# Kernel tuning notes

Hardware: AMD Instinct MI355X
Metric: run time of the kernel (lower is better)

Reference implementation:

```python
import jax, jax.numpy as jnp
import numpy as np

L, H, D, HD, DFF, V, S, B = 12, 12, 768, 64, 3072, 50257, 512, 4
NEG = -1e10  # mask value used by the torch module (applied incl. diagonal, pre-scale)


def layer_norm(x, g, b, eps=1e-5):
    u = jnp.mean(x, axis=-1, keepdims=True)
    v = jnp.mean((x - u) ** 2, axis=-1, keepdims=True)  # biased variance
    return g * (x - u) / jnp.sqrt(v + eps) + b


def setup_inputs() -> dict:
    key = jax.random.key(0)
    ks = jax.random.split(key, 10)
    f = lambda k, s: 0.02 * jax.random.normal(k, s, dtype=jnp.float32)
    return {
        "tokens": jax.random.randint(ks[0], (B, S), 0, V),
        "E": f(ks[1], (V, D)),
        "P": f(ks[2], (S, D)),
        "Wq": f(ks[3], (L, H, HD, D)),
        "Wk": f(ks[4], (L, H, HD, D)),
        "Wv": f(ks[5], (L, H, HD, D)),
        "Wo": f(ks[6], (L, D, D)),
        "bo": jnp.zeros((L, D), jnp.float32),
        "g1": jnp.ones((L, D), jnp.float32),
        "b1": jnp.zeros((L, D), jnp.float32),
        "g2": jnp.ones((L, D), jnp.float32),
        "b2": jnp.zeros((L, D), jnp.float32),
        "W1": f(ks[7], (L, DFF, D)),
        "bff1": jnp.zeros((L, DFF), jnp.float32),
        "W2": f(ks[8], (L, D, DFF)),
        "bff2": jnp.zeros((L, D), jnp.float32),
        "gf": jnp.ones((D,), jnp.float32),
        "bf": jnp.zeros((D,), jnp.float32),
    }


def reference(tokens, E, P, Wq, Wk, Wv, Wo, bo, g1, b1, g2, b2, W1, bff1, W2, bff2, gf, bf):
    x = E[tokens] + P[None, :, :]  # [B,S,D]; embed_dropout is identity at eval
    # Faithful mask: triu with diagonal=0 (masks the diagonal too), added BEFORE 1/sqrt(dk)
    mask = jnp.triu(jnp.ones((S, S), jnp.float32), k=0) * NEG
    scale = 1.0 / jnp.sqrt(jnp.float32(HD))
    for l in range(L):
        h = layer_norm(x, g1[l], b1[l])
        Q = jnp.einsum('bsd,hkd->bhsk', h, Wq[l])
        K = jnp.einsum('bsd,hkd->bhsk', h, Wk[l])
        Vh = jnp.einsum('bsd,hkd->bhsk', h, Wv[l])
        sc = (jnp.einsum('bhqk,bhmk->bhqm', Q, K) + mask) * scale  # [B,H,S,S]
        A = jax.nn.softmax(sc, axis=-1)
        o = jnp.einsum('bhqm,bhmk->bhqk', A, Vh)  # [B,H,S,HD]
        o = o.transpose(0, 2, 1, 3).reshape(B, S, D)  # concat heads
        x = x + jnp.einsum('bsd,ed->bse', o, Wo[l]) + bo[l]
        h2 = layer_norm(x, g2[l], b2[l])
        ff = jax.nn.gelu(jnp.einsum('bsd,fd->bsf', h2, W1[l]) + bff1[l], approximate=False)
        x = x + jnp.einsum('bsf,df->bsd', ff, W2[l]) + bff2[l]
    x = layer_norm(x, gf, bf)
    return jnp.einsum('bsd,vd->bsv', x, E)  # weight-tied LM head
```

## Files before the change

kernel.cpp:

```cpp
#include <hip/hip_runtime.h>
#include <hip/hip_bf16.h>
#include <math.h>
#include <stdint.h>

#define L      12
#define H      12
#define DMODEL 768
#define HDIM   64
#define DFF    3072
#define VOCAB  50257
#define VPAD2  50432
#define SEQ    512
#define BATCH  4
#define MTOK   2048
#define BKK    64

typedef __hip_bfloat16 bf16;
typedef __bf16 bf16x8 __attribute__((ext_vector_type(8)));
typedef float  f32x4  __attribute__((ext_vector_type(4)));

__device__ inline unsigned int f2bf_bits(float f) {
    __hip_bfloat16 h = __float2bfloat16(f);
    return (unsigned int)__builtin_bit_cast(unsigned short, h);
}

typedef __attribute__((address_space(1))) unsigned int as1_uint;
typedef __attribute__((address_space(3))) unsigned int as3_uint;

__device__ inline void load_lds_16B(const void* g, void* l) {
    __builtin_amdgcn_global_load_lds((as1_uint*)(uintptr_t)g,
                                     (as3_uint*)(uintptr_t)l, 16, 0, 0);
}

__device__ inline int xcd_swz(int raw, int nwg) {
    return (raw & 7) * (nwg >> 3) + (raw >> 3);
}

struct CvtP {
    const float* src[7];
    bf16* dst[7];
    long ns[7];
    long nt[7];
};

__global__ void cvt_all_kernel(CvtP c) {
    long gid0 = ((long)blockIdx.x * blockDim.x + threadIdx.x) * 8;
    long gstr = (long)gridDim.x * blockDim.x * 8;
    for (int s = 0; s < 7; s++) {
        const float* src = c.src[s];
        bf16* dst = c.dst[s];
        long ns = c.ns[s], ntt = c.nt[s];
        for (long i8 = gid0; i8 < ntt; i8 += gstr) {
            uint4 out;
            if (i8 < ns) {
                float4 a = *reinterpret_cast<const float4*>(src + i8);
                float4 b = *reinterpret_cast<const float4*>(src + i8 + 4);
                out.x = f2bf_bits(a.x) | (f2bf_bits(a.y) << 16);
                out.y = f2bf_bits(a.z) | (f2bf_bits(a.w) << 16);
                out.z = f2bf_bits(b.x) | (f2bf_bits(b.y) << 16);
                out.w = f2bf_bits(b.z) | (f2bf_bits(b.w) << 16);
            } else {
                out = (uint4){0u, 0u, 0u, 0u};
            }
            *reinterpret_cast<uint4*>(dst + i8) = out;
        }
    }
}

__global__ __launch_bounds__(256) void embed_ln_kernel(
        float* __restrict__ x, bf16* __restrict__ hout,
        const int* __restrict__ tok, const float* __restrict__ E,
        const float* __restrict__ Pp, const float* __restrict__ g,
        const float* __restrict__ b) {
    int wave = threadIdx.x >> 6, lane = threadIdx.x & 63;
    int row = blockIdx.x * 4 + wave;
    int s = row & (SEQ - 1);
    long ebase = (long)tok[row] * 192;
    const float4* E4 = (const float4*)E;
    const float4* P4 = (const float4*)Pp;
    float4 v[3];
    float s1 = 0.f, s2 = 0.f;
    #pragma unroll
    for (int e = 0; e < 3; e++) {
        int c4 = e * 64 + lane;
        float4 a = E4[ebase + c4];
        float4 p = P4[s * 192 + c4];
        a.x += p.x; a.y += p.y; a.z += p.z; a.w += p.w;
        v[e] = a;
        ((float4*)x)[(size_t)row * 192 + c4] = a;
        s1 += a.x + a.y + a.z + a.w;
        s2 += a.x * a.x + a.y * a.y + a.z * a.z + a.w * a.w;
    }
    #pragma unroll
    for (int o = 32; o > 0; o >>= 1) {
        s1 += __shfl_xor(s1, o);
        s2 += __shfl_xor(s2, o);
    }
    float u    = s1 * (1.f / DMODEL);
    float var  = s2 * (1.f / DMODEL) - u * u;
    float rstd = rsqrtf(var + 1e-5f);
    #pragma unroll
    for (int e = 0; e < 3; e++) {
        int c4 = e * 64 + lane;
        float4 gg = ((const float4*)g)[c4];
        float4 bb = ((const float4*)b)[c4];
        float y0 = gg.x * (v[e].x - u) * rstd + bb.x;
        float y1 = gg.y * (v[e].y - u) * rstd + bb.y;
        float y2 = gg.z * (v[e].z - u) * rstd + bb.z;
        float y3 = gg.w * (v[e].w - u) * rstd + bb.w;
        uint2 o2;
        o2.x = f2bf_bits(y0) | (f2bf_bits(y1) << 16);
        o2.y = f2bf_bits(y2) | (f2bf_bits(y3) << 16);
        ((uint2*)hout)[(size_t)row * 192 + c4] = o2;
    }
}

__global__ __launch_bounds__(256) void ln_kernel(
        const float* __restrict__ x, const float* __restrict__ g,
        const float* __restrict__ b, bf16* __restrict__ hout) {
    int wave = threadIdx.x >> 6, lane = threadIdx.x & 63;
    int row = blockIdx.x * 4 + wave;
    float4 v[3];
    float s1 = 0.f, s2 = 0.f;
    #pragma unroll
    for (int e = 0; e < 3; e++) {
        int c4 = e * 64 + lane;
        float4 a = ((const float4*)x)[(size_t)row * 192 + c4];
        v[e] = a;
        s1 += a.x + a.y + a.z + a.w;
        s2 += a.x * a.x + a.y * a.y + a.z * a.z + a.w * a.w;
    }
    #pragma unroll
    for (int o = 32; o > 0; o >>= 1) {
        s1 += __shfl_xor(s1, o);
        s2 += __shfl_xor(s2, o);
    }
    float u    = s1 * (1.f / DMODEL);
    float var  = s2 * (1.f / DMODEL) - u * u;
    float rstd = rsqrtf(var + 1e-5f);
    #pragma unroll
    for (int e = 0; e < 3; e++) {
        int c4 = e * 64 + lane;
        float4 gg = ((const float4*)g)[c4];
        float4 bb = ((const float4*)b)[c4];
        float y0 = gg.x * (v[e].x - u) * rstd + bb.x;
        float y1 = gg.y * (v[e].y - u) * rstd + bb.y;
        float y2 = gg.z * (v[e].z - u) * rstd + bb.z;
        float y3 = gg.w * (v[e].w - u) * rstd + bb.w;
        uint2 o2;
        o2.x = f2bf_bits(y0) | (f2bf_bits(y1) << 16);
        o2.y = f2bf_bits(y2) | (f2bf_bits(y3) << 16);
        ((uint2*)hout)[(size_t)row * 192 + c4] = o2;
    }
}

#define BM 128

template<int BN_, int EPI>
__global__ __launch_bounds__(256) void gemm_bt(
    const bf16* __restrict__ A, const bf16* __restrict__ Bmat, long strideBz,
    void* __restrict__ Cout, long strideCz,
    const float* __restrict__ bias,
    int Mm, int Nn, int Kk, int Nstore)
{
    constexpr int NF = BN_ / 32;
    __shared__ __align__(16) bf16 As[2][BM * BKK];
    __shared__ __align__(16) bf16 Bs[2][BN_ * BKK];
    int tid = threadIdx.x;
    int lane = tid & 63, wave = tid >> 6;

    int Mtiles = Mm / BM;
    int id = xcd_swz(blockIdx.x, gridDim.x);
    int bm = (id % Mtiles) * BM;
    int bn = (id / Mtiles) * BN_;
    int z = blockIdx.z;
    const bf16* Bz = Bmat + (size_t)z * strideBz;
    int wr = (wave >> 1) * 64, wc = (wave & 1) * (BN_ / 2);

    int nt = Kk / BKK;

    f32x4 acc[4][NF];
    #pragma unroll
    for (int i = 0; i < 4; i++)
        #pragma unroll
        for (int j = 0; j < NF; j++) acc[i][j] = (f32x4){0.f, 0.f, 0.f, 0.f};

    auto stage = [&](int slot, int kt) {
        #pragma unroll
        for (int i = 0; i < 4; i++) {
            int byte = i * 4096 + tid * 16;
            int r = byte >> 7;
            int scb = (byte & 127) ^ ((r & 7) << 4);
            load_lds_16B(A + (size_t)(bm + r) * Kk + kt + (scb >> 1),
                         (char*)As[slot] + byte);
        }
        #pragma unroll
        for (int i = 0; i < BN_ / 32; i++) {
            int byte = i * 4096 + tid * 16;
            int r = byte >> 7;
            int scb = (byte & 127) ^ ((r & 7) << 4);
            load_lds_16B(Bz + (size_t)(bn + r) * Kk + kt + (scb >> 1),
                         (char*)Bs[slot] + byte);
        }
    };

    const int swz_rd = (lane & 7) << 4;
    stage(0, 0);
    for (int t = 0; t < nt; ++t) {
        if (t + 1 < nt) {
            stage((t + 1) & 1, (t + 1) * BKK);
            if constexpr (BN_ == 128) {
                asm volatile("s_waitcnt vmcnt(8)" ::: "memory");
            } else {
                asm volatile("s_waitcnt vmcnt(6)" ::: "memory");
            }
        } else {
            asm volatile("s_waitcnt vmcnt(0)" ::: "memory");
        }
        __builtin_amdgcn_s_barrier();
        __builtin_amdgcn_sched_barrier(0);
        __builtin_amdgcn_s_setprio(1);
        int cur = t & 1;
        #pragma unroll
        for (int kk = 0; kk < 2; ++kk) {
            bf16x8 af[4], bfr[NF];
            int ro = lane & 15;
            int cob = kk * 64 + (lane >> 4) * 16;
            #pragma unroll
            for (int mi = 0; mi < 4; mi++) {
                int row = wr + mi * 16 + ro;
                af[mi] = *reinterpret_cast<const bf16x8*>(
                    (const char*)As[cur] + row * 128 + (cob ^ swz_rd));
            }
            #pragma unroll
            for (int ni = 0; ni < NF; ni++) {
                int row = wc + ni * 16 + ro;
                bfr[ni] = *reinterpret_cast<const bf16x8*>(
                    (const char*)Bs[cur] + row * 128 + (cob ^ swz_rd));
            }
            #pragma unroll
            for (int mi = 0; mi < 4; mi++)
                #pragma unroll
                for (int ni = 0; ni < NF; ni++)
                    acc[mi][ni] = __builtin_amdgcn_mfma_f32_16x16x32_bf16(
                        af[mi], bfr[ni], acc[mi][ni], 0, 0, 0);
        }
        __builtin_amdgcn_s_setprio(0);
        __builtin_amdgcn_s_barrier();
    }

    int rbase = bm + wr + ((lane >> 4) << 2);
    int cbase = bn + wc + (lane & 15);
    #pragma unroll
    for (int mi = 0; mi < 4; mi++) {
        #pragma unroll
        for (int ni = 0; ni < NF; ni++) {
            int col = cbase + ni * 16;
            #pragma unroll
            for (int r = 0; r < 4; r++) {
                int row = rbase + mi * 16 + r;
                float v = acc[mi][ni][r];
                if constexpr (EPI == 0) {
                    ((bf16*)Cout)[(size_t)z * strideCz + (size_t)row * Nn + col] =
                        __float2bfloat16(v);
                } else if constexpr (EPI == 1) {
                    size_t idx = (size_t)row * Nn + col;
                    float* resid = (float*)Cout;
                    resid[idx] = resid[idx] + v + bias[col];
                } else if constexpr (EPI == 2) {
                    float t2 = v + bias[col];
                    float gel = 0.5f * t2 * (1.f + erff(t2 * 0.70710678118654752f));
                    ((bf16*)Cout)[(size_t)row * Nn + col] = __float2bfloat16(gel);
                } else {
                    if (col < Nstore)
                        ((float*)Cout)[(size_t)row * Nstore + col] = v;
                }
            }
        }
    }
}

#define NEGMASK -1e10f
#define SM_SCALE 0.125f

__global__ __launch_bounds__(256) void attn_kernel(
    bf16* __restrict__ o, const bf16* __restrict__ qb,
    const bf16* __restrict__ kb, const bf16* __restrict__ vb)
{
    __shared__ __align__(16) bf16 K_lds[64 * 64];
    __shared__ __align__(16) bf16 VT_lds[64 * 64];
    __shared__ __align__(16) bf16 P_lds[4][16 * 64];

    int tid = threadIdx.x;
    int wave = tid >> 6, lane = tid & 63;
    int g = lane >> 4;
    int cq = lane & 15;
    int idx = xcd_swz(blockIdx.x, gridDim.x);
    int qt = idx & 7;
    int bh = idx >> 3;
    int h = bh % H, b = bh / H;
    int q0 = qt * 64;
    const size_t base = ((size_t)b * SEQ) * DMODEL + h * HDIM;

    bf16x8 qa[2];
    #pragma unroll
    for (int kk = 0; kk < 2; kk++)
        qa[kk] = *reinterpret_cast<const bf16x8*>(
            qb + base + (size_t)(q0 + wave * 16 + cq) * DMODEL + kk * 32 + g * 8);

    f32x4 acc_o[4];
    #pragma unroll
    for (int df = 0; df < 4; df++) acc_o[df] = (f32x4){0.f, 0.f, 0.f, 0.f};
    float m_run[4] = {-INFINITY, -INFINITY, -INFINITY, -INFINITY};
    float l_run[4] = {0.f, 0.f, 0.f, 0.f};

    int ntiles = (qt == 0) ? (SEQ / 64) : (qt + 1);
    for (int t = 0; t < ntiles; ++t) {
        int mt = t * 64;
        __syncthreads();
        #pragma unroll
        for (int i = 0; i < 2; i++) {
            int byte = i * 4096 + tid * 16;
            int r = byte >> 7;
            int scb = (byte & 127) ^ ((r & 7) << 4);
            load_lds_16B(kb + base + (size_t)(mt + r) * DMODEL + (scb >> 1),
                         (char*)K_lds + byte);
        }
        {
            int rp = tid & 31;
            int c0 = (tid >> 5) * 8;
            const bf16* v0p = vb + base + (size_t)(mt + 2 * rp) * DMODEL + c0;
            uint4 a = *reinterpret_cast<const uint4*>(v0p);
            uint4 bb = *reinterpret_cast<const uint4*>(v0p + DMODEL);
            unsigned int au[4] = {a.x, a.y, a.z, a.w};
            unsigned int bu[4] = {bb.x, bb.y, bb.z, bb.w};
            #pragma unroll
            for (int j = 0; j < 8; j++) {
                unsigned int lo = (j & 1) ? (au[j >> 1] >> 16) : (au[j >> 1] & 0xffffu);
                unsigned int hi = (j & 1) ? (bu[j >> 1] >> 16) : (bu[j >> 1] & 0xffffu);
                int d = c0 + j;
                int byte = d * 128 + ((rp * 4) ^ ((d & 7) << 4));
                *reinterpret_cast<unsigned int*>((char*)VT_lds + byte) = lo | (hi << 16);
            }
        }
        __syncthreads();

        f32x4 s[4];
        #pragma unroll
        for (int nf = 0; nf < 4; nf++) s[nf] = (f32x4){0.f, 0.f, 0.f, 0.f};
        __builtin_amdgcn_s_setprio(1);
        #pragma unroll
        for (int kk = 0; kk < 2; kk++) {
            #pragma unroll
            for (int nf = 0; nf < 4; nf++) {
                int row = nf * 16 + cq;
                bf16x8 kf = *reinterpret_cast<const bf16x8*>(
                    (const char*)K_lds + row * 128 +
                    ((kk * 64 + g * 16) ^ ((row & 7) << 4)));
                s[nf] = __builtin_amdgcn_mfma_f32_16x16x32_bf16(qa[kk], kf, s[nf], 0, 0, 0);
            }
        }
        __builtin_amdgcn_s_setprio(0);

        float p[4][4];
        #pragma unroll
        for (int r = 0; r < 4; r++) {
            int qg = q0 + wave * 16 + (g << 2) + r;
            float sv[4];
            float vmax = -INFINITY;
            #pragma unroll
            for (int nf = 0; nf < 4; nf++) {
                int kv = mt + nf * 16 + cq;
                float d = s[nf][r];
                sv[nf] = (kv >= qg) ? (d + NEGMASK) * SM_SCALE : d * SM_SCALE;
                vmax = fmaxf(vmax, sv[nf]);
            }
            vmax = fmaxf(vmax, __shfl_xor(vmax, 1));
            vmax = fmaxf(vmax, __shfl_xor(vmax, 2));
            vmax = fmaxf(vmax, __shfl_xor(vmax, 4));
            vmax = fmaxf(vmax, __shfl_xor(vmax, 8));
            float nm = fmaxf(m_run[r], vmax);
            float f = __expf(m_run[r] - nm);
            m_run[r] = nm;
            float ps = 0.f;
            #pragma unroll
            for (int nf = 0; nf < 4; nf++) {
                float pv = __expf(sv[nf] - nm);
                p[nf][r] = pv;
                ps += pv;
            }
            ps += __shfl_xor(ps, 1);
            ps += __shfl_xor(ps, 2);
            ps += __shfl_xor(ps, 4);
            ps += __shfl_xor(ps, 8);
            l_run[r] = l_run[r] * f + ps;
            #pragma unroll
            for (int df = 0; df < 4; df++) acc_o[df][r] *= f;
        }

        #pragma unroll
        for (int nf = 0; nf < 4; nf++)
            #pragma unroll
            for (int r = 0; r < 4; r++) {
                int q = (g << 2) + r;
                int blog = nf * 32 + cq * 2;
                int byte = wave * 2048 + q * 128 + (blog ^ ((q & 7) << 4));
                *reinterpret_cast<unsigned short*>((char*)P_lds + byte) =
                    (unsigned short)f2bf_bits(p[nf][r]);
            }
        __syncthreads();

        __builtin_amdgcn_s_setprio(1);
        #pragma unroll
        for (int kk = 0; kk < 2; kk++) {
            bf16x8 pa = *reinterpret_cast<const bf16x8*>(
                (const char*)P_lds + wave * 2048 + cq * 128 +
                ((kk * 64 + g * 16) ^ ((cq & 7) << 4)));
            #pragma unroll
            for (int df = 0; df < 4; df++) {
                int row = df * 16 + cq;
                bf16x8 vf = *reinterpret_cast<const bf16x8*>(
                    (const char*)VT_lds + row * 128 +
                    ((kk * 64 + g * 16) ^ ((row & 7) << 4)));
                acc_o[df] = __builtin_amdgcn_mfma_f32_16x16x32_bf16(pa, vf, acc_o[df], 0, 0, 0);
            }
        }
        __builtin_amdgcn_s_setprio(0);
    }

    #pragma unroll
    for (int r = 0; r < 4; r++) {
        float inv = 1.f / l_run[r];
        int qg = q0 + wave * 16 + (g << 2) + r;
        #pragma unroll
        for (int df = 0; df < 4; df++) {
            o[base + (size_t)qg * DMODEL + df * 16 + cq] =
                __float2bfloat16(acc_o[df][r] * inv);
        }
    }
}

extern "C" void kernel_launch(void* const* d_in, const int* in_sizes, int n_in,
                              void* d_out, int out_size, void* d_ws, size_t ws_size,
                              hipStream_t stream)
{
    (void)in_sizes; (void)n_in; (void)out_size; (void)ws_size;
    const int*   tokens = (const int*)d_in[0];
    const float* E    = (const float*)d_in[1];
    const float* P    = (const float*)d_in[2];
    const float* Wq   = (const float*)d_in[3];
    const float* Wk   = (const float*)d_in[4];
    const float* Wv   = (const float*)d_in[5];
    const float* Wo   = (const float*)d_in[6];
    const float* bo   = (const float*)d_in[7];
    const float* g1   = (const float*)d_in[8];
    const float* b1   = (const float*)d_in[9];
    const float* g2   = (const float*)d_in[10];
    const float* b2   = (const float*)d_in[11];
    const float* W1   = (const float*)d_in[12];
    const float* bff1 = (const float*)d_in[13];
    const float* W2   = (const float*)d_in[14];
    const float* bff2 = (const float*)d_in[15];
    const float* gf   = (const float*)d_in[16];
    const float* bfin = (const float*)d_in[17];

    char* ws = (char*)d_ws;
    size_t off = 0;
    auto alloc = [&](size_t bytes) -> void* {
        void* p = ws + off;
        off += (bytes + 255) & ~(size_t)255;
        return p;
    };
    float* x     = (float*)alloc((size_t)MTOK * DMODEL * 4);
    bf16* hbuf   = (bf16*)alloc((size_t)MTOK * DMODEL * 2);
    bf16* qkv    = (bf16*)alloc((size_t)3 * MTOK * DMODEL * 2);
    bf16* obuf   = (bf16*)alloc((size_t)MTOK * DMODEL * 2);
    bf16* ffb    = (bf16*)alloc((size_t)MTOK * DFF * 2);
    bf16* Eb     = (bf16*)alloc((size_t)VPAD2 * DMODEL * 2);
    bf16* Wqkv_b = (bf16*)alloc((size_t)3 * L * DMODEL * DMODEL * 2);
    bf16* Wo_b   = (bf16*)alloc((size_t)L * DMODEL * DMODEL * 2);
    bf16* W1_b   = (bf16*)alloc((size_t)L * DFF * DMODEL * 2);
    bf16* W2_b   = (bf16*)alloc((size_t)L * DMODEL * DFF * 2);

    long nW = (long)L * DMODEL * DMODEL;
    long nF = (long)L * DFF * DMODEL;
    CvtP cp;
    cp.src[0] = E;  cp.dst[0] = Eb;          cp.ns[0] = (long)VOCAB * DMODEL; cp.nt[0] = (long)VPAD2 * DMODEL;
    cp.src[1] = Wq; cp.dst[1] = Wqkv_b;      cp.ns[1] = nW; cp.nt[1] = nW;
    cp.src[2] = Wk; cp.dst[2] = Wqkv_b + nW; cp.ns[2] = nW; cp.nt[2] = nW;
    cp.src[3] = Wv; cp.dst[3] = Wqkv_b + 2 * nW; cp.ns[3] = nW; cp.nt[3] = nW;
    cp.src[4] = Wo; cp.dst[4] = Wo_b;        cp.ns[4] = nW; cp.nt[4] = nW;
    cp.src[5] = W1; cp.dst[5] = W1_b;        cp.ns[5] = nF; cp.nt[5] = nF;
    cp.src[6] = W2; cp.dst[6] = W2_b;        cp.ns[6] = nF; cp.nt[6] = nF;
    cvt_all_kernel<<<2048, 256, 0, stream>>>(cp);

    embed_ln_kernel<<<MTOK / 4, 256, 0, stream>>>(x, hbuf, tokens, E, P, g1, b1);

    const long pstride = (long)MTOK * DMODEL;
    for (int l = 0; l < L; ++l) {
        gemm_bt<64, 0><<<dim3(192, 1, 3), 256, 0, stream>>>(
            hbuf, Wqkv_b + (size_t)l * DMODEL * DMODEL, nW,
            qkv, pstride, nullptr, MTOK, DMODEL, DMODEL, 0);
        attn_kernel<<<BATCH * H * (SEQ / 64), 256, 0, stream>>>(
            obuf, qkv, qkv + pstride, qkv + 2 * pstride);
        gemm_bt<64, 1><<<dim3(192, 1, 1), 256, 0, stream>>>(
            obuf, Wo_b + (size_t)l * DMODEL * DMODEL, 0,
            x, 0, bo + l * DMODEL, MTOK, DMODEL, DMODEL, 0);
        ln_kernel<<<MTOK / 4, 256, 0, stream>>>(
            x, g2 + l * DMODEL, b2 + l * DMODEL, hbuf);
        gemm_bt<128, 2><<<dim3(16 * 24, 1, 1), 256, 0, stream>>>(
            hbuf, W1_b + (size_t)l * DFF * DMODEL, 0,
            ffb, 0, bff1 + l * DFF, MTOK, DFF, DMODEL, 0);
        gemm_bt<64, 1><<<dim3(192, 1, 1), 256, 0, stream>>>(
            ffb, W2_b + (size_t)l * DMODEL * DFF, 0,
            x, 0, bff2 + l * DMODEL, MTOK, DMODEL, DFF, 0);
        const float* ng = (l < L - 1) ? (g1 + (l + 1) * DMODEL) : gf;
        const float* nb = (l < L - 1) ? (b1 + (l + 1) * DMODEL) : bfin;
        ln_kernel<<<MTOK / 4, 256, 0, stream>>>(x, ng, nb, hbuf);
    }
    gemm_bt<128, 3><<<dim3(16 * 394, 1, 1), 256, 0, stream>>>(
        hbuf, Eb, 0, d_out, 0, nullptr, MTOK, VPAD2, DMODEL, VOCAB);
}
```

Before: 1.849 ms.

## Split-K the Wo/W2 GEMMs with fused reduce+LN, add 256x128 LM-head kernel

The Wo and W2 projection GEMMs now use split-K over three slices, each writing fp32 partials. A new reduce_ln_kernel sums those partials with the bias and residual, writes x, and computes the following layer norm. This triples the block count on the small-N GEMMs, which previously ran only 192 blocks, at the cost of extra fp32 partial traffic. Separately, the LM head uses a new 512-thread 256x128-tile kernel with a three-stage LDS pipeline and 144KB of dynamic shared memory, falling back to the old kernel if the launch fails.

```diff
diff --git a/kernel.cpp b/kernel.cpp
--- a/kernel.cpp
+++ b/kernel.cpp
@@ -115,18 +115,28 @@
     }
 }
 
-__global__ __launch_bounds__(256) void ln_kernel(
-        const float* __restrict__ x, const float* __restrict__ g,
+__global__ __launch_bounds__(256) void reduce_ln_kernel(
+        float* __restrict__ x, const float* __restrict__ part, int S,
+        const float* __restrict__ bias, const float* __restrict__ g,
         const float* __restrict__ b, bf16* __restrict__ hout) {
     int wave = threadIdx.x >> 6, lane = threadIdx.x & 63;
     int row = blockIdx.x * 4 + wave;
+    const float4* part4 = (const float4*)part;
     float4 v[3];
     float s1 = 0.f, s2 = 0.f;
     #pragma unroll
     for (int e = 0; e < 3; e++) {
         int c4 = e * 64 + lane;
-        float4 a = ((const float4*)x)[(size_t)row * 192 + c4];
+        size_t idx = (size_t)row * 192 + c4;
+        float4 a = ((const float4*)x)[idx];
+        float4 bi = ((const float4*)bias)[c4];
+        a.x += bi.x; a.y += bi.y; a.z += bi.z; a.w += bi.w;
+        for (int sl = 0; sl < S; sl++) {
+            float4 p = part4[((size_t)sl * MTOK + row) * 192 + c4];
+            a.x += p.x; a.y += p.y; a.z += p.z; a.w += p.w;
+        }
         v[e] = a;
+        ((float4*)x)[idx] = a;
         s1 += a.x + a.y + a.z + a.w;
         s2 += a.x * a.x + a.y * a.y + a.z * a.z + a.w * a.w;
     }
@@ -161,7 +171,7 @@
     const bf16* __restrict__ A, const bf16* __restrict__ Bmat, long strideBz,
     void* __restrict__ Cout, long strideCz,
     const float* __restrict__ bias,
-    int Mm, int Nn, int Kk, int Nstore)
+    int Mm, int Nn, int Kk, int Nstore, int kslice)
 {
     constexpr int NF = BN_ / 32;
     __shared__ __align__(16) bf16 As[2][BM * BKK];
@@ -177,7 +187,8 @@
     const bf16* Bz = Bmat + (size_t)z * strideBz;
     int wr = (wave >> 1) * 64, wc = (wave & 1) * (BN_ / 2);
 
-    int nt = Kk / BKK;
+    int k0 = (EPI == 4) ? z * kslice : 0;
+    int nt = ((EPI == 4) ? kslice : Kk) / BKK;
 
     f32x4 acc[4][NF];
     #pragma unroll
@@ -205,10 +216,10 @@
     };
 
     const int swz_rd = (lane & 7) << 4;
-    stage(0, 0);
+    stage(0, k0);
     for (int t = 0; t < nt; ++t) {
         if (t + 1 < nt) {
-            stage((t + 1) & 1, (t + 1) * BKK);
+            stage((t + 1) & 1, k0 + (t + 1) * BKK);
             if constexpr (BN_ == 128) {
                 asm volatile("s_waitcnt vmcnt(8)" ::: "memory");
             } else {
@@ -263,18 +274,115 @@
                 if constexpr (EPI == 0) {
                     ((bf16*)Cout)[(size_t)z * strideCz + (size_t)row * Nn + col] =
                         __float2bfloat16(v);
-                } else if constexpr (EPI == 1) {
-                    size_t idx = (size_t)row * Nn + col;
-                    float* resid = (float*)Cout;
-                    resid[idx] = resid[idx] + v + bias[col];
                 } else if constexpr (EPI == 2) {
                     float t2 = v + bias[col];
                     float gel = 0.5f * t2 * (1.f + erff(t2 * 0.70710678118654752f));
                     ((bf16*)Cout)[(size_t)row * Nn + col] = __float2bfloat16(gel);
-                } else {
+                } else if constexpr (EPI == 3) {
                     if (col < Nstore)
                         ((float*)Cout)[(size_t)row * Nstore + col] = v;
+                } else {
+                    ((float*)Cout)[(size_t)z * strideCz + (size_t)row * Nn + col] = v;
                 }
+            }
+        }
+    }
+}
+
+__global__ void __launch_bounds__(512, 2) gemm_head256(
+    const bf16* __restrict__ A, const bf16* __restrict__ Bmat,
+    float* __restrict__ Cout, int Nstore)
+{
+    extern __shared__ char smem[];
+    const int Kk = DMODEL;
+    const int nt = Kk / BKK;
+    int tid = threadIdx.x;
+    int lane = tid & 63, wave = tid >> 6;
+    int wm = wave >> 1, wn = wave & 1;
+    int id = xcd_swz(blockIdx.x, gridDim.x);
+    int bm = (id & 7) * 256;
+    int bn = (id >> 3) * 128;
+
+    f32x4 acc[4][4];
+    #pragma unroll
+    for (int i = 0; i < 4; i++)
+        #pragma unroll
+        for (int j = 0; j < 4; j++) acc[i][j] = (f32x4){0.f, 0.f, 0.f, 0.f};
+
+    auto stage = [&](int slot, int kt) {
+        #pragma unroll
+        for (int i = 0; i < 4; i++) {
+            int byte = i * 8192 + tid * 16;
+            int r = byte >> 7;
+            int scb = (byte & 127) ^ ((r & 7) << 4);
+            load_lds_16B(A + (size_t)(bm + r) * Kk + kt + (scb >> 1),
+                         smem + slot * 32768 + byte);
+        }
+        #pragma unroll
+        for (int i = 0; i < 2; i++) {
+            int byte = i * 8192 + tid * 16;
+            int r = byte >> 7;
+            int scb = (byte & 127) ^ ((r & 7) << 4);
+            load_lds_16B(Bmat + (size_t)(bn + r) * Kk + kt + (scb >> 1),
+                         smem + 98304 + slot * 16384 + byte);
+        }
+    };
+
+    const int swz_rd = (lane & 7) << 4;
+    stage(0, 0);
+    stage(1, BKK);
+    for (int t = 0; t < nt; ++t) {
+        if (t < nt - 1) {
+            asm volatile("s_waitcnt vmcnt(6)" ::: "memory");
+        } else {
+            asm volatile("s_waitcnt vmcnt(0)" ::: "memory");
+        }
+        __builtin_amdgcn_s_barrier();
+        __builtin_amdgcn_sched_barrier(0);
+        if (t + 2 < nt) stage((t + 2) % 3, (t + 2) * BKK);
+        int cur = t % 3;
+        const char* Ab = smem + cur * 32768;
+        const char* Bb = smem + 98304 + cur * 16384;
+        __builtin_amdgcn_s_setprio(1);
+        #pragma unroll
+        for (int kk = 0; kk < 2; ++kk) {
+            bf16x8 af[4], bfr[4];
+            int ro = lane & 15;
+            int cob = kk * 64 + (lane >> 4) * 16;
+            #pragma unroll
+            for (int mi = 0; mi < 4; mi++) {
+                int row = wm * 64 + mi * 16 + ro;
+                af[mi] = *reinterpret_cast<const bf16x8*>(
+                    Ab + row * 128 + (cob ^ swz_rd));
+            }
+            #pragma unroll
+            for (int ni = 0; ni < 4; ni++) {
+                int row = wn * 64 + ni * 16 + ro;
+                bfr[ni] = *reinterpret_cast<const bf16x8*>(
+                    Bb + row * 128 + (cob ^ swz_rd));
+            }
+            #pragma unroll
+            for (int mi = 0; mi < 4; mi++)
+                #pragma unroll
+                for (int ni = 0; ni < 4; ni++)
+                    acc[mi][ni] = __builtin_amdgcn_mfma_f32_16x16x32_bf16(
+                        af[mi], bfr[ni], acc[mi][ni], 0, 0, 0);
+        }
+        __builtin_amdgcn_s_setprio(0);
+    }
+
+    int rbase = bm + wm * 64 + ((lane >> 4) << 2);
+    int cbase = bn + wn * 64 + (lane & 15);
+    #pragma unroll
+    for (int mi = 0; mi < 4; mi++) {
+        #pragma unroll
+        for (int ni = 0; ni < 4; ni++) {
+            int col = cbase + ni * 16;
+            #pragma unroll
+            for (int r = 0; r < 4; r++) {
+                int row = rbase + mi * 16 + r;
+                if (col < Nstore)
+                    Cout[(size_t)row * Nstore + col] = acc[mi][ni][r];
             }
         }
     }
@@ -476,6 +584,7 @@
     bf16* qkv    = (bf16*)alloc((size_t)3 * MTOK * DMODEL * 2);
     bf16* obuf   = (bf16*)alloc((size_t)MTOK * DMODEL * 2);
     bf16* ffb    = (bf16*)alloc((size_t)MTOK * DFF * 2);
+    float* part  = (float*)alloc((size_t)3 * MTOK * DMODEL * 4);
     bf16* Eb     = (bf16*)alloc((size_t)VPAD2 * DMODEL * 2);
     bf16* Wqkv_b = (bf16*)alloc((size_t)3 * L * DMODEL * DMODEL * 2);
     bf16* Wo_b   = (bf16*)alloc((size_t)L * DMODEL * DMODEL * 2);
@@ -500,24 +609,33 @@
     for (int l = 0; l < L; ++l) {
         gemm_bt<64, 0><<<dim3(192, 1, 3), 256, 0, stream>>>(
             hbuf, Wqkv_b + (size_t)l * DMODEL * DMODEL, nW,
-            qkv, pstride, nullptr, MTOK, DMODEL, DMODEL, 0);
+            qkv, pstride, nullptr, MTOK, DMODEL, DMODEL, 0, 0);
         attn_kernel<<<BATCH * H * (SEQ / 64), 256, 0, stream>>>(
             obuf, qkv, qkv + pstride, qkv + 2 * pstride);
-        gemm_bt<64, 1><<<dim3(192, 1, 1), 256, 0, stream>>>(
+        gemm_bt<64, 4><<<dim3(192, 1, 3), 256, 0, stream>>>(
             obuf, Wo_b + (size_t)l * DMODEL * DMODEL, 0,
-            x, 0, bo + l * DMODEL, MTOK, DMODEL, DMODEL, 0);
-        ln_kernel<<<MTOK / 4, 256, 0, stream>>>(
-            x, g2 + l * DMODEL, b2 + l * DMODEL, hbuf);
+            part, pstride, nullptr, MTOK, DMODEL, DMODEL, 0, DMODEL / 3);
+        reduce_ln_kernel<<<MTOK / 4, 256, 0, stream>>>(
+            x, part, 3, bo + l * DMODEL, g2 + l * DMODEL, b2 + l * DMODEL, hbuf);
         gemm_bt<128, 2><<<dim3(16 * 24, 1, 1), 256, 0, stream>>>(
             hbuf, W1_b + (size_t)l * DFF * DMODEL, 0,
-            ffb, 0, bff1 + l * DFF, MTOK, DFF, DMODEL, 0);
-        gemm_bt<64, 1><<<dim3(192, 1, 1), 256, 0, stream>>>(
+            ffb, 0, bff1 + l * DFF, MTOK, DFF, DMODEL, 0, 0);
+        gemm_bt<64, 4><<<dim3(192, 1, 3), 256, 0, stream>>>(
             ffb, W2_b + (size_t)l * DMODEL * DFF, 0,
-            x, 0, bff2 + l * DMODEL, MTOK, DMODEL, DFF, 0);
+            part, pstride, nullptr, MTOK, DMODEL, DFF, 0, DFF / 3);
         const float* ng = (l < L - 1) ? (g1 + (l + 1) * DMODEL) : gf;
         const float* nb = (l < L - 1) ? (b1 + (l + 1) * DMODEL) : bfin;
-        ln_kernel<<<MTOK / 4, 256, 0, stream>>>(x, ng, nb, hbuf);
-    }
-    gemm_bt<128, 3><<<dim3(16 * 394, 1, 1), 256, 0, stream>>>(
-        hbuf, Eb, 0, d_out, 0, nullptr, MTOK, VPAD2, DMODEL, VOCAB);
-}
+        reduce_ln_kernel<<<MTOK / 4, 256, 0, stream>>>(
+            x, part, 3, bff2 + l * DMODEL, ng, nb, hbuf);
+    }
+
+    (void)hipFuncSetAttribute((const void*)gemm_head256,
+        hipFuncAttributeMaxDynamicSharedMemorySize, 147456);
+    (void)hipGetLastError();
+    gemm_head256<<<dim3(8 * 394), 512, 147456, stream>>>(
+        hbuf, Eb, (float*)d_out, VOCAB);
+    if (hipGetLastError() != hipSuccess) {
+        gemm_bt<128, 3><<<dim3(16 * 394, 1, 1), 256, 0, stream>>>(
+            hbuf, Eb, 0, d_out, 0, nullptr, MTOK, VPAD2, DMODEL, VOCAB, 0);
+    }
+}
```

Measured after the change: 1.740 ms. 1.06x faster.
